# Optimization experiments

Measured on AMD Instinct MI355X. Metric: run time of the kernel, lower is better.

Reference implementation:

```python
import jax, jax.numpy as jnp
import numpy as np

B, S, E, H = 2, 2048, 1024, 16
D = E // H  # head_dim = 64

def setup_inputs() -> dict:
    key = jax.random.key(0)
    ks = jax.random.split(key, 5)
    scale = 0.02
    return {
        "x": jax.random.normal(ks[0], (B, S, E), dtype=jnp.float32),
        "Wq": jax.random.normal(ks[1], (E, E), dtype=jnp.float32) * scale,
        "Wk": jax.random.normal(ks[2], (E, E), dtype=jnp.float32) * scale,
        "Wv": jax.random.normal(ks[3], (E, E), dtype=jnp.float32) * scale,
        "Wo": jax.random.normal(ks[4], (E, E), dtype=jnp.float32) * scale,
        "bo": jnp.zeros((E,), dtype=jnp.float32),
    }

def reference(x, Wq, Wk, Wv, Wo, bo):
    b, s, e = x.shape
    # Linear projections (torch Linear: x @ W.T), split heads -> (b, h, s, d)
    q = (x @ Wq.T).reshape(b, s, H, D).transpose(0, 2, 1, 3)
    k = (x @ Wk.T).reshape(b, s, H, D).transpose(0, 2, 1, 3)
    v = (x @ Wv.T).reshape(b, s, H, D).transpose(0, 2, 1, 3)
    # Full materialized causal scores (b, h, s, s)
    scores = jnp.einsum("bhqd,bhkd->bhqk", q, k)
    causal = jnp.tril(jnp.ones((s, s), dtype=bool))  # True = keep
    scores = jnp.where(causal, scores, -jnp.inf)
    attn = jax.nn.softmax(scores / jnp.sqrt(jnp.float32(D)), axis=-1)
    ctx = jnp.einsum("bhqk,bhkd->bhqd", attn, v)
    ctx = ctx.transpose(0, 2, 1, 3).reshape(b, s, e)
    return ctx @ Wo.T + bo
```

## Files before the change

kernel.cpp:

```cpp
#include <hip/hip_runtime.h>
#include <hip/hip_bf16.h>

typedef __attribute__((ext_vector_type(8))) short short8_t;
typedef __attribute__((ext_vector_type(4))) short s4v;
typedef __attribute__((ext_vector_type(4))) float f32x4_t;
typedef __attribute__((ext_vector_type(4))) unsigned u32x4_t;
using u16 = unsigned short;

constexpr int S_LEN = 2048;
constexpr int EMB   = 1024;
constexpr int NH    = 16;
constexpr int HD    = 64;
constexpr int BATCH = 2;
constexpr int MR    = BATCH * S_LEN;
constexpr int E3    = 3 * EMB;

#define L2E 1.44269504f

__device__ __forceinline__ u16 f2bf(float f) {
  unsigned u = __builtin_bit_cast(unsigned, f);
  unsigned r = 0x7fffu + ((u >> 16) & 1u);
  return (u16)((u + r) >> 16);
}

__device__ __forceinline__ unsigned pkbf(float a, float b) {
  __hip_bfloat162 h = __float22bfloat162_rn(make_float2(a, b));
  unsigned u;
  __builtin_memcpy(&u, &h, 4);
  return u;
}

__device__ __forceinline__ void gld16(const void* g, void* l) {
  __builtin_amdgcn_global_load_lds(
      (const __attribute__((address_space(1))) void*)g,
      (__attribute__((address_space(3))) void*)l, 16, 0, 0);
}

template <int OFF>
__device__ __forceinline__ s4v tr16(const __attribute__((address_space(3))) u16* p) {
  s4v d;
  asm volatile("ds_read_b64_tr_b16 %0, %1 offset:%2"
               : "=v"(d) : "v"(p), "n"(OFF));
  return d;
}

__global__ void k_cvt_all(const float* __restrict__ x, const float* __restrict__ Wq,
                          const float* __restrict__ Wk, const float* __restrict__ Wv,
                          const float* __restrict__ Wo, u16* __restrict__ out) {
  int i = blockIdx.x * 256 + threadIdx.x;
  const float* src;
  int j;
  float sc = 1.0f;
  if (i < (1 << 20)) {
    src = x; j = i;
  } else {
    int jj = i - (1 << 20);
    int r = jj >> 18;
    j = jj & ((1 << 18) - 1);
    src = (r == 0) ? Wq : (r == 1) ? Wk : (r == 2) ? Wv : Wo;
    if (r == 0) sc = 0.125f;
  }
  float4 v = reinterpret_cast<const float4*>(src)[j];
  ushort4 o;
  o.x = f2bf(v.x * sc); o.y = f2bf(v.y * sc);
  o.z = f2bf(v.z * sc); o.w = f2bf(v.w * sc);
  reinterpret_cast<ushort4*>(out)[i] = o;
}

template <bool F32OUT>
__global__ __launch_bounds__(256) void k_gemm_bt(
    const u16* __restrict__ A, const u16* __restrict__ Bw,
    void* __restrict__ Cv, const float* __restrict__ bias,
    int M, int N, int K) {
  __shared__ short As[2][128 * 32];
  __shared__ short Bs[2][128 * 32];
  const int t    = threadIdx.x;
  const int w    = t >> 6;
  const int ln15 = t & 15;
  const int lg   = (t >> 4) & 3;
  const int wr   = w >> 1, wc = w & 1;

  const int nwgx = gridDim.x;
  const int lin  = blockIdx.y * nwgx + blockIdx.x;
  const int cpx  = (nwgx * gridDim.y) >> 3;
  const int lin2 = (lin & 7) * cpx + (lin >> 3);
  const int m0   = (lin2 / nwgx) * 128;
  const int n0   = (lin2 % nwgx) * 128;

  const int srow = t >> 2;
  const int scol = (t & 3) * 8;
  const u16* gA = A + (size_t)(m0 + srow) * K + scol;
  const u16* gB = Bw + (size_t)(n0 + srow) * K + scol;
  const int lofs = w * 512;

  f32x4_t acc[4][4] = {};

#define GSTAGE(buf, k0)                                                        \
  do {                                                                         \
    gld16(gA + (k0), &As[buf][lofs]);                                          \
    gld16(gA + (size_t)64 * K + (k0), &As[buf][lofs + 2048]);                  \
    gld16(gB + (k0), &Bs[buf][lofs]);                                          \
    gld16(gB + (size_t)64 * K + (k0), &Bs[buf][lofs + 2048]);                  \
  } while (0)

  const int nk = K >> 5;
  GSTAGE(0, 0);
  int cur = 0;

  for (int ki = 0; ki < nk; ++ki) {
    asm volatile("s_barrier" ::: "memory");
    if (ki + 1 < nk) {
      GSTAGE(cur ^ 1, (ki + 1) * 32);
      asm volatile("s_waitcnt vmcnt(4)" ::: "memory");
    } else {
      asm volatile("s_waitcnt vmcnt(0)" ::: "memory");
    }
    asm volatile("s_barrier" ::: "memory");

    short8_t af[4], bf[4];
#pragma unroll
    for (int i = 0; i < 4; ++i) {
      af[i] = *reinterpret_cast<const short8_t*>(
          &As[cur][(wr * 64 + i * 16 + ln15) * 32 + 8 * lg]);
      bf[i] = *reinterpret_cast<const short8_t*>(
          &Bs[cur][(wc * 64 + i * 16 + ln15) * 32 + 8 * lg]);
    }
#pragma unroll
    for (int i = 0; i < 4; ++i)
#pragma unroll
      for (int j = 0; j < 4; ++j)
        acc[i][j] = __builtin_amdgcn_mfma_f32_16x16x32_bf16(
            af[i], bf[j], acc[i][j], 0, 0, 0);
    cur ^= 1;
  }
#undef GSTAGE

  if (F32OUT) {
    float* C = reinterpret_cast<float*>(Cv);
#pragma unroll
    for (int i = 0; i < 4; ++i)
#pragma unroll
      for (int j = 0; j < 4; ++j) {
        const int col = n0 + wc * 64 + j * 16 + ln15;
        const float bv = bias ? bias[col] : 0.0f;
#pragma unroll
        for (int r = 0; r < 4; ++r) {
          const int row = m0 + wr * 64 + i * 16 + lg * 4 + r;
          C[(size_t)row * N + col] = acc[i][j][r] + bv;
        }
      }
  } else {
    u16* C = reinterpret_cast<u16*>(Cv);
#pragma unroll
    for (int i = 0; i < 4; ++i)
#pragma unroll
      for (int j = 0; j < 4; ++j) {
        const int col = n0 + wc * 64 + j * 16 + ln15;
#pragma unroll
        for (int r = 0; r < 4; ++r) {
          const int row = m0 + wr * 64 + i * 16 + lg * 4 + r;
          C[(size_t)row * N + col] = f2bf(acc[i][j][r]);
        }
      }
  }
}

__global__ __launch_bounds__(256, 4) void k_attn2(const u16* __restrict__ QKV,
                                                  u16* __restrict__ ctx) {
  __shared__ u16 Ks[2][64 * 64];
  __shared__ u16 Vs[2][64 * 64];

  const int t    = threadIdx.x;
  const int w    = t >> 6;
  const int l    = t & 63;
  const int ln15 = t & 15;
  const int lg   = (l >> 4) & 3;

  const int qt = 31 - blockIdx.y;
  const int bh = blockIdx.x;
  const int b  = bh >> 4, h = bh & 15;

  const u16* KVb = QKV + (size_t)b * S_LEN * E3 + h * HD;
  const u16* Kg  = KVb + 1024;
  const u16* Vg  = KVb + 2048;
  const int qrow = qt * 64 + w * 16;

  short8_t qf[2];
  {
    const u16* qp = KVb + (size_t)(qrow + ln15) * E3 + 8 * lg;
    qf[0] = *reinterpret_cast<const short8_t*>(qp);
    qf[1] = *reinterpret_cast<const short8_t*>(qp + 32);
  }

  const int krow_lo = l >> 3;
  const int kcol    = 8 * ((l & 7) ^ krow_lo);
  const int vkv     = l >> 1;
  const int vcol    = 16 * w + 8 * (l & 1);

  const int kx  = 8 * (ln15 & 7);
  const int kc0 = (8 * lg) ^ kx;
  const int kc1 = (32 + 8 * lg) ^ kx;

#define STAGE(buf, kv0)                                                        \
  do {                                                                         \
    gld16(Kg + (size_t)((kv0) + 16 * w + krow_lo) * E3 + kcol,                 \
          &Ks[buf][1024 * w]);                                                 \
    gld16(Kg + (size_t)((kv0) + 16 * w + 8 + krow_lo) * E3 + kcol,             \
          &Ks[buf][1024 * w + 512]);                                           \
    gld16(Vg + (size_t)((kv0) + vkv) * E3 + vcol, &Vs[buf][1024 * w]);         \
    gld16(Vg + (size_t)((kv0) + 32 + vkv) * E3 + vcol,                         \
          &Vs[buf][1024 * w + 512]);                                           \
  } while (0)

  f32x4_t o[4] = {};
  float mrow = -3e38f, lrow = 0.0f;
  const int nt_tiles = qt + 1;

  STAGE(0, 0);
  int cur = 0;

  for (int kvt = 0; kvt < nt_tiles; ++kvt) {
    const int kv0 = kvt * 64;
    asm volatile("s_barrier" ::: "memory");
    if (kvt + 1 < nt_tiles) {
      STAGE(cur ^ 1, kv0 + 64);
      asm volatile("s_waitcnt vmcnt(4)" ::: "memory");
    } else {
      asm volatile("s_waitcnt vmcnt(0)" ::: "memory");
    }
    asm volatile("s_barrier" ::: "memory");

    const __attribute__((address_space(3))) u16* vp =
        (const __attribute__((address_space(3))) u16*)&Vs[cur][4 * l];
    s4v vf[4][2][2];
#pragma unroll
    for (int nt = 0; nt < 4; ++nt) {
      if (nt == 0) { vf[0][0][0]=tr16<0>(vp);    vf[0][0][1]=tr16<512>(vp);
                     vf[0][1][0]=tr16<1024>(vp); vf[0][1][1]=tr16<1536>(vp); }
      if (nt == 1) { vf[1][0][0]=tr16<2048>(vp); vf[1][0][1]=tr16<2560>(vp);
                     vf[1][1][0]=tr16<3072>(vp); vf[1][1][1]=tr16<3584>(vp); }
      if (nt == 2) { vf[2][0][0]=tr16<4096>(vp); vf[2][0][1]=tr16<4608>(vp);
                     vf[2][1][0]=tr16<5120>(vp); vf[2][1][1]=tr16<5632>(vp); }
      if (nt == 3) { vf[3][0][0]=tr16<6144>(vp); vf[3][0][1]=tr16<6656>(vp);
                     vf[3][1][0]=tr16<7168>(vp); vf[3][1][1]=tr16<7680>(vp); }
    }

    f32x4_t tacc[4];
    __builtin_amdgcn_s_setprio(1);
#pragma unroll
    for (int ks = 0; ks < 4; ++ks) {
      const int R = 16 * ks + ln15;
      short8_t kf0 = *reinterpret_cast<const short8_t*>(&Ks[cur][R * 64 + kc0]);
      short8_t kf1 = *reinterpret_cast<const short8_t*>(&Ks[cur][R * 64 + kc1]);
      f32x4_t a = {0.f, 0.f, 0.f, 0.f};
      a = __builtin_amdgcn_mfma_f32_16x16x32_bf16(kf0, qf[0], a, 0, 0, 0);
      a = __builtin_amdgcn_mfma_f32_16x16x32_bf16(kf1, qf[1], a, 0, 0, 0);
      tacc[ks] = a;
    }
    __builtin_amdgcn_s_setprio(0);

    if (kvt == qt) {
      const int qg = qrow + ln15;
#pragma unroll
      for (int ks = 0; ks < 4; ++ks)
#pragma unroll
        for (int r = 0; r < 4; ++r)
          if (kv0 + 16 * ks + 4 * lg + r > qg) tacc[ks][r] = -3e38f;
    }

    float rm = fmaxf(
        fmaxf(fmaxf(fmaxf(tacc[0][0], tacc[0][1]), fmaxf(tacc[0][2], tacc[0][3])),
              fmaxf(fmaxf(tacc[1][0], tacc[1][1]), fmaxf(tacc[1][2], tacc[1][3]))),
        fmaxf(fmaxf(fmaxf(tacc[2][0], tacc[2][1]), fmaxf(tacc[2][2], tacc[2][3])),
              fmaxf(fmaxf(tacc[3][0], tacc[3][1]), fmaxf(tacc[3][2], tacc[3][3]))));
    rm = fmaxf(rm, __shfl_xor(rm, 16, 64));
    rm = fmaxf(rm, __shfl_xor(rm, 32, 64));

    if (__any(rm > mrow)) {
      const float nm = fmaxf(mrow, rm);
      const float sc = exp2f((mrow - nm) * L2E);
      mrow = nm;
      lrow *= sc;
#pragma unroll
      for (int r = 0; r < 4; ++r) {
        const float so = __shfl(sc, 20 * lg + r, 64);
#pragma unroll
        for (int nt = 0; nt < 4; ++nt) o[nt][r] *= so;
      }
    }

    const float nmL = mrow * L2E;
    float p[4][4];
    float rs = 0.0f;
#pragma unroll
    for (int ks = 0; ks < 4; ++ks)
#pragma unroll
      for (int r = 0; r < 4; ++r) {
        const float pv = exp2f(fmaf(tacc[ks][r], L2E, -nmL));
        p[ks][r] = pv;
        rs += pv;
      }
    rs += __shfl_xor(rs, 16, 64);
    rs += __shfl_xor(rs, 32, 64);
    lrow += rs;

    short8_t pf[2];
#pragma unroll
    for (int s2 = 0; s2 < 2; ++s2) {
      u32x4_t pu;
      pu[0] = pkbf(p[2 * s2][0], p[2 * s2][1]);
      pu[1] = pkbf(p[2 * s2][2], p[2 * s2][3]);
      pu[2] = pkbf(p[2 * s2 + 1][0], p[2 * s2 + 1][1]);
      pu[3] = pkbf(p[2 * s2 + 1][2], p[2 * s2 + 1][3]);
      pf[s2] = __builtin_bit_cast(short8_t, pu);
    }

    asm volatile("s_waitcnt lgkmcnt(0)");
    __builtin_amdgcn_sched_barrier(0);

    __builtin_amdgcn_s_setprio(1);
#pragma unroll
    for (int nt = 0; nt < 4; ++nt) {
#pragma unroll
      for (int s2 = 0; s2 < 2; ++s2) {
        short8_t bv = __builtin_shufflevector(vf[nt][s2][0], vf[nt][s2][1],
                                              0, 1, 2, 3, 4, 5, 6, 7);
        o[nt] = __builtin_amdgcn_mfma_f32_16x16x32_bf16(pf[s2], bv, o[nt], 0, 0, 0);
      }
    }
    __builtin_amdgcn_s_setprio(0);
    cur ^= 1;
  }
#undef STAGE

  const float linv = 1.0f / lrow;
#pragma unroll
  for (int r = 0; r < 4; ++r) {
    const float li = __shfl(linv, 20 * lg + r, 64);
    u16* op = ctx + (size_t)(b * S_LEN + qrow + 4 * lg + r) * EMB + h * HD;
#pragma unroll
    for (int nt = 0; nt < 4; ++nt)
      op[nt * 16 + ln15] = f2bf(o[nt][r] * li);
  }
}

extern "C" void kernel_launch(void* const* d_in, const int* in_sizes, int n_in,
                              void* d_out, int out_size, void* d_ws, size_t ws_size,
                              hipStream_t stream) {
  const float* x  = (const float*)d_in[0];
  const float* Wq = (const float*)d_in[1];
  const float* Wk = (const float*)d_in[2];
  const float* Wv = (const float*)d_in[3];
  const float* Wo = (const float*)d_in[4];
  const float* bo = (const float*)d_in[5];

  u16* ws   = (u16*)d_ws;
  u16* xb   = ws;
  u16* wcat = xb + (size_t)MR * EMB;
  u16* wob  = wcat + (size_t)3 * EMB * EMB;
  u16* qkv  = wob + (size_t)EMB * EMB;
  u16* ctxb = qkv + (size_t)MR * E3;

  k_cvt_all<<<8192, 256, 0, stream>>>(x, Wq, Wk, Wv, Wo, xb);

  k_gemm_bt<false><<<dim3(E3 / 128, MR / 128), 256, 0, stream>>>(
      xb, wcat, qkv, nullptr, MR, E3, EMB);

  k_attn2<<<dim3(BATCH * NH, 32), 256, 0, stream>>>(qkv, ctxb);

  k_gemm_bt<true><<<dim3(EMB / 128, MR / 128), 256, 0, stream>>>(
      ctxb, wob, d_out, bo, MR, EMB, EMB);
}
```

Baseline: 117.6 us.

## Process two KV tiles per iteration with a shared softmax rescale

Restructures the causal attention loop so each iteration loads and processes two 64-row KV tiles, computing a joint row max and rescaling the output once per 128 keys instead of once per 64. This roughly halves the per-tile softmax bookkeeping (max reduction shuffles, rescale of o) and the barrier count. It drops the double-buffered prefetch: both tiles are loaded and then waited on fully with vmcnt(0) before compute, so global loads no longer overlap compute. This exposes memory latency and adds register pressure from the second score tile.

Measured after the change: 122.1 us. 3.8% more time.

```diff
diff --git a/kernel.cpp b/kernel.cpp
--- a/kernel.cpp
+++ b/kernel.cpp
@@ -184,6 +184,7 @@
   const u16* Kg  = KVb + 1024;
   const u16* Vg  = KVb + 2048;
   const int qrow = qt * 64 + w * 16;
+  const int qg   = qrow + ln15;
 
   short8_t qf[2];
   {
@@ -212,67 +213,118 @@
           &Vs[buf][1024 * w + 512]);                                           \
   } while (0)
 
+#define VTRREAD(vf, buf)                                                       \
+  do {                                                                         \
+    const __attribute__((address_space(3))) u16* vp =                          \
+        (const __attribute__((address_space(3))) u16*)&Vs[buf][4 * l];         \
+    vf[0][0][0]=tr16<0>(vp);    vf[0][0][1]=tr16<512>(vp);                     \
+    vf[0][1][0]=tr16<1024>(vp); vf[0][1][1]=tr16<1536>(vp);                    \
+    vf[1][0][0]=tr16<2048>(vp); vf[1][0][1]=tr16<2560>(vp);                    \
+    vf[1][1][0]=tr16<3072>(vp); vf[1][1][1]=tr16<3584>(vp);                    \
+    vf[2][0][0]=tr16<4096>(vp); vf[2][0][1]=tr16<4608>(vp);                    \
+    vf[2][1][0]=tr16<5120>(vp); vf[2][1][1]=tr16<5632>(vp);                    \
+    vf[3][0][0]=tr16<6144>(vp); vf[3][0][1]=tr16<6656>(vp);                    \
+    vf[3][1][0]=tr16<7168>(vp); vf[3][1][1]=tr16<7680>(vp);                    \
+  } while (0)
+
+#define QKTILE(tacc, buf)                                                      \
+  do {                                                                         \
+    _Pragma("unroll")                                                          \
+    for (int ks = 0; ks < 4; ++ks) {                                           \
+      const int R = 16 * ks + ln15;                                            \
+      short8_t kf0 = *reinterpret_cast<const short8_t*>(&Ks[buf][R * 64 + kc0]);\
+      short8_t kf1 = *reinterpret_cast<const short8_t*>(&Ks[buf][R * 64 + kc1]);\
+      f32x4_t a = {0.f, 0.f, 0.f, 0.f};                                        \
+      a = __builtin_amdgcn_mfma_f32_16x16x32_bf16(kf0, qf[0], a, 0, 0, 0);     \
+      a = __builtin_amdgcn_mfma_f32_16x16x32_bf16(kf1, qf[1], a, 0, 0, 0);     \
+      tacc[ks] = a;                                                            \
+    }                                                                          \
+  } while (0)
+
+#define MASK(tacc, kvb)                                                        \
+  do {                                                                         \
+    _Pragma("unroll")                                                          \
+    for (int ks = 0; ks < 4; ++ks)                                             \
+      _Pragma("unroll")                                                        \
+      for (int r = 0; r < 4; ++r)                                              \
+        if ((kvb) + 16 * ks + 4 * lg + r > qg) tacc[ks][r] = -3e38f;           \
+  } while (0)
+
+#define EXPP(p, tacc)                                                          \
+  do {                                                                         \
+    _Pragma("unroll")                                                          \
+    for (int ks = 0; ks < 4; ++ks)                                             \
+      _Pragma("unroll")                                                        \
+      for (int r = 0; r < 4; ++r) {                                            \
+        const float pv = exp2f(fmaf(tacc[ks][r], L2E, -nmL));                  \
+        p[ks][r] = pv;                                                         \
+        rs += pv;                                                              \
+      }                                                                        \
+  } while (0)
+
+#define PACK(pf, p)                                                            \
+  do {                                                                         \
+    _Pragma("unroll")                                                          \
+    for (int s2 = 0; s2 < 2; ++s2) {                                           \
+      u32x4_t pu;                                                              \
+      pu[0] = pkbf(p[2 * s2][0], p[2 * s2][1]);                                \
+      pu[1] = pkbf(p[2 * s2][2], p[2 * s2][3]);                                \
+      pu[2] = pkbf(p[2 * s2 + 1][0], p[2 * s2 + 1][1]);                        \
+      pu[3] = pkbf(p[2 * s2 + 1][2], p[2 * s2 + 1][3]);                        \
+      pf[s2] = __builtin_bit_cast(short8_t, pu);                               \
+    }                                                                          \
+  } while (0)
+
+#define PV(pf, vf)                                                             \
+  do {                                                                         \
+    _Pragma("unroll")                                                          \
+    for (int nt = 0; nt < 4; ++nt)                                             \
+      _Pragma("unroll")                                                        \
+      for (int s2 = 0; s2 < 2; ++s2) {                                         \
+        short8_t bv = __builtin_shufflevector(vf[nt][s2][0], vf[nt][s2][1],    \
+                                              0, 1, 2, 3, 4, 5, 6, 7);         \
+        o[nt] = __builtin_amdgcn_mfma_f32_16x16x32_bf16(pf[s2], bv, o[nt],     \
+                                                        0, 0, 0);              \
+      }                                                                        \
+  } while (0)
+
   f32x4_t o[4] = {};
   float mrow = -3e38f, lrow = 0.0f;
-  const int nt_tiles = qt + 1;
-
-  STAGE(0, 0);
-  int cur = 0;
-
-  for (int kvt = 0; kvt < nt_tiles; ++kvt) {
-    const int kv0 = kvt * 64;
+
+  for (int kv0 = 0; kv0 <= qt * 64; kv0 += 128) {
+    const int t0   = kv0 >> 6;
+    const bool two = (t0 + 1 <= qt);
+
     asm volatile("s_barrier" ::: "memory");
-    if (kvt + 1 < nt_tiles) {
-      STAGE(cur ^ 1, kv0 + 64);
-      asm volatile("s_waitcnt vmcnt(4)" ::: "memory");
-    } else {
-      asm volatile("s_waitcnt vmcnt(0)" ::: "memory");
-    }
+    STAGE(0, kv0);
+    if (two) STAGE(1, kv0 + 64);
+    asm volatile("s_waitcnt vmcnt(0)" ::: "memory");
     asm volatile("s_barrier" ::: "memory");
 
-    const __attribute__((address_space(3))) u16* vp =
-        (const __attribute__((address_space(3))) u16*)&Vs[cur][4 * l];
-    s4v vf[4][2][2];
-#pragma unroll
-    for (int nt = 0; nt < 4; ++nt) {
-      if (nt == 0) { vf[0][0][0]=tr16<0>(vp);    vf[0][0][1]=tr16<512>(vp);
-                     vf[0][1][0]=tr16<1024>(vp); vf[0][1][1]=tr16<1536>(vp); }
-      if (nt == 1) { vf[1][0][0]=tr16<2048>(vp); vf[1][0][1]=tr16<2560>(vp);
-                     vf[1][1][0]=tr16<3072>(vp); vf[1][1][1]=tr16<3584>(vp); }
-      if (nt == 2) { vf[2][0][0]=tr16<4096>(vp); vf[2][0][1]=tr16<4608>(vp);
-                     vf[2][1][0]=tr16<5120>(vp); vf[2][1][1]=tr16<5632>(vp); }
-      if (nt == 3) { vf[3][0][0]=tr16<6144>(vp); vf[3][0][1]=tr16<6656>(vp);
-                     vf[3][1][0]=tr16<7168>(vp); vf[3][1][1]=tr16<7680>(vp); }
-    }
-
-    f32x4_t tacc[4];
+    s4v vfA[4][2][2];
+    VTRREAD(vfA, 0);
+
+    f32x4_t ta[4], tb[4];
     __builtin_amdgcn_s_setprio(1);
-#pragma unroll
-    for (int ks = 0; ks < 4; ++ks) {
-      const int R = 16 * ks + ln15;
-      short8_t kf0 = *reinterpret_cast<const short8_t*>(&Ks[cur][R * 64 + kc0]);
-      short8_t kf1 = *reinterpret_cast<const short8_t*>(&Ks[cur][R * 64 + kc1]);
-      f32x4_t a = {0.f, 0.f, 0.f, 0.f};
-      a = __builtin_amdgcn_mfma_f32_16x16x32_bf16(kf0, qf[0], a, 0, 0, 0);
-      a = __builtin_amdgcn_mfma_f32_16x16x32_bf16(kf1, qf[1], a, 0, 0, 0);
-      tacc[ks] = a;
-    }
+    QKTILE(ta, 0);
+    if (two) QKTILE(tb, 1);
     __builtin_amdgcn_s_setprio(0);
 
-    if (kvt == qt) {
-      const int qg = qrow + ln15;
-#pragma unroll
-      for (int ks = 0; ks < 4; ++ks)
-#pragma unroll
-        for (int r = 0; r < 4; ++r)
-          if (kv0 + 16 * ks + 4 * lg + r > qg) tacc[ks][r] = -3e38f;
-    }
+    if (!two) MASK(ta, kv0);
+    if (two && (t0 + 1 == qt)) MASK(tb, kv0 + 64);
 
     float rm = fmaxf(
-        fmaxf(fmaxf(fmaxf(tacc[0][0], tacc[0][1]), fmaxf(tacc[0][2], tacc[0][3])),
-              fmaxf(fmaxf(tacc[1][0], tacc[1][1]), fmaxf(tacc[1][2], tacc[1][3]))),
-        fmaxf(fmaxf(fmaxf(tacc[2][0], tacc[2][1]), fmaxf(tacc[2][2], tacc[2][3])),
-              fmaxf(fmaxf(tacc[3][0], tacc[3][1]), fmaxf(tacc[3][2], tacc[3][3]))));
+        fmaxf(fmaxf(fmaxf(ta[0][0], ta[0][1]), fmaxf(ta[0][2], ta[0][3])),
+              fmaxf(fmaxf(ta[1][0], ta[1][1]), fmaxf(ta[1][2], ta[1][3]))),
+        fmaxf(fmaxf(fmaxf(ta[2][0], ta[2][1]), fmaxf(ta[2][2], ta[2][3])),
+              fmaxf(fmaxf(ta[3][0], ta[3][1]), fmaxf(ta[3][2], ta[3][3]))));
+    if (two) {
+      rm = fmaxf(rm, fmaxf(
+          fmaxf(fmaxf(fmaxf(tb[0][0], tb[0][1]), fmaxf(tb[0][2], tb[0][3])),
+                fmaxf(fmaxf(tb[1][0], tb[1][1]), fmaxf(tb[1][2], tb[1][3]))),
+          fmaxf(fmaxf(fmaxf(tb[2][0], tb[2][1]), fmaxf(tb[2][2], tb[2][3])),
+                fmaxf(fmaxf(tb[3][0], tb[3][1]), fmaxf(tb[3][2], tb[3][3])))));
+    }
     rm = fmaxf(rm, __shfl_xor(rm, 16, 64));
     rm = fmaxf(rm, __shfl_xor(rm, 32, 64));
 
@@ -290,48 +342,44 @@
     }
 
     const float nmL = mrow * L2E;
-    float p[4][4];
     float rs = 0.0f;
-#pragma unroll
-    for (int ks = 0; ks < 4; ++ks)
-#pragma unroll
-      for (int r = 0; r < 4; ++r) {
-        const float pv = exp2f(fmaf(tacc[ks][r], L2E, -nmL));
-        p[ks][r] = pv;
-        rs += pv;
-      }
+    float pA[4][4];
+    EXPP(pA, ta);
+    short8_t pfA[2];
+    PACK(pfA, pA);
+    short8_t pfB[2];
+    if (two) {
+      float pB[4][4];
+      EXPP(pB, tb);
+      PACK(pfB, pB);
+    }
     rs += __shfl_xor(rs, 16, 64);
     rs += __shfl_xor(rs, 32, 64);
     lrow += rs;
 
-    short8_t pf[2];
-#pragma unroll
-    for (int s2 = 0; s2 < 2; ++s2) {
-      u32x4_t pu;
-      pu[0] = pkbf(p[2 * s2][0], p[2 * s2][1]);
-      pu[1] = pkbf(p[2 * s2][2], p[2 * s2][3]);
-      pu[2] = pkbf(p[2 * s2 + 1][0], p[2 * s2 + 1][1]);
-      pu[3] = pkbf(p[2 * s2 + 1][2], p[2 * s2 + 1][3]);
-      pf[s2] = __builtin_bit_cast(short8_t, pu);
-    }
-
     asm volatile("s_waitcnt lgkmcnt(0)");
     __builtin_amdgcn_sched_barrier(0);
-
     __builtin_amdgcn_s_setprio(1);
-#pragma unroll
-    for (int nt = 0; nt < 4; ++nt) {
-#pragma unroll
-      for (int s2 = 0; s2 < 2; ++s2) {
-        short8_t bv = __builtin_shufflevector(vf[nt][s2][0], vf[nt][s2][1],
-                                              0, 1, 2, 3, 4, 5, 6, 7);
-        o[nt] = __builtin_amdgcn_mfma_f32_16x16x32_bf16(pf[s2], bv, o[nt], 0, 0, 0);
-      }
-    }
+    PV(pfA, vfA);
     __builtin_amdgcn_s_setprio(0);
-    cur ^= 1;
+
+    if (two) {
+      s4v vfB[4][2][2];
+      VTRREAD(vfB, 1);
+      asm volatile("s_waitcnt lgkmcnt(0)");
+      __builtin_amdgcn_sched_barrier(0);
+      __builtin_amdgcn_s_setprio(1);
+      PV(pfB, vfB);
+      __builtin_amdgcn_s_setprio(0);
+    }
   }
 #undef STAGE
+#undef VTRREAD
+#undef QKTILE
+#undef MASK
+#undef EXPP
+#undef PACK
+#undef PV
 
   const float linv = 1.0f / lrow;
 #pragma unroll
```

## Use 256x256-tile 512-thread GEMM kernel for QKV projection

Applied to the files above, without the earlier changes.

Adds a new bf16 MFMA GEMM kernel with 256x256 output tiles, 8 waves, K-step 64 and double-buffered LDS with XOR swizzle, and uses it for the fused QKV projection instead of the 128x128 kernel. Larger tiles raise arithmetic intensity and cut global/L2 traffic per FLOP. The cost is a 12x16=192-workgroup grid, which gives lower occupancy (one block per CU, 128KB LDS) and may under-fill the CUs. It also carries a large register footprint from the 32 accumulators per lane.

After: 119.7 us. No clear change (+1.9%).

```diff
diff --git a/kernel.cpp b/kernel.cpp
--- a/kernel.cpp
+++ b/kernel.cpp
@@ -67,6 +67,103 @@
   reinterpret_cast<ushort4*>(out)[i] = o;
 }
 
+__global__ __launch_bounds__(512, 1) void k_gemm256(
+    const u16* __restrict__ A, const u16* __restrict__ Bw,
+    u16* __restrict__ C, int M, int N) {
+  constexpr int K = 1024;
+  __shared__ u16 Ab[2][16384];
+  __shared__ u16 Bb[2][16384];
+
+  const int t    = threadIdx.x;
+  const int ww   = t >> 6;
+  const int l    = t & 63;
+  const int ln15 = t & 15;
+  const int lg   = (t >> 4) & 3;
+  const int wr   = ww >> 2;
+  const int wc   = ww & 3;
+
+  const int nwgx = gridDim.x;
+  const int lin  = blockIdx.y * nwgx + blockIdx.x;
+  const int cpx  = (nwgx * gridDim.y) >> 3;
+  const int lin2 = (lin & 7) * cpx + (lin >> 3);
+  const int m0   = (lin2 / nwgx) * 256;
+  const int n0   = (lin2 % nwgx) * 256;
+
+  const int srow = t >> 3;
+  const int rlo  = (t >> 3) & 7;
+  const int scol = 8 * ((t & 7) ^ rlo);
+
+  const int kx  = 8 * (ln15 & 7);
+  const int kc0 = (8 * lg) ^ kx;
+  const int kc1 = (32 + 8 * lg) ^ kx;
+
+  f32x4_t acc[8][4] = {};
+
+#define GST256(buf, ki)                                                        \
+  do {                                                                         \
+    _Pragma("unroll")                                                          \
+    for (int i = 0; i < 4; ++i)                                                \
+      gld16(A + (size_t)(m0 + 64 * i + srow) * K + 64 * (ki) + scol,           \
+            &Ab[buf][i * 4096 + ww * 512]);                                    \
+    _Pragma("unroll")                                                          \
+    for (int i = 0; i < 4; ++i)                                                \
+      gld16(Bw + (size_t)(n0 + 64 * i + srow) * K + 64 * (ki) + scol,          \
+            &Bb[buf][i * 4096 + ww * 512]);                                    \
+  } while (0)
+
+  constexpr int nk = K / 64;
+  GST256(0, 0);
+  int cur = 0;
+
+  for (int ki = 0; ki < nk; ++ki) {
+    asm volatile("s_barrier" ::: "memory");
+    if (ki + 1 < nk) {
+      GST256(cur ^ 1, ki + 1);
+      asm volatile("s_waitcnt vmcnt(8)" ::: "memory");
+    } else {
+      asm volatile("s_waitcnt vmcnt(0)" ::: "memory");
+    }
+    asm volatile("s_barrier" ::: "memory");
+
+#pragma unroll
+    for (int kh = 0; kh < 2; ++kh) {
+      const int kc = kh ? kc1 : kc0;
+      short8_t af[8], bf[4];
+#pragma unroll
+      for (int mi = 0; mi < 8; ++mi)
+        af[mi] = *reinterpret_cast<const short8_t*>(
+            &Ab[cur][(wr * 128 + 16 * mi + ln15) * 64 + kc]);
+#pragma unroll
+      for (int ni = 0; ni < 4; ++ni)
+        bf[ni] = *reinterpret_cast<const short8_t*>(
+            &Bb[cur][(wc * 64 + 16 * ni + ln15) * 64 + kc]);
+      __builtin_amdgcn_s_setprio(1);
+#pragma unroll
+      for (int mi = 0; mi < 8; ++mi)
+#pragma unroll
+        for (int ni = 0; ni < 4; ++ni)
+          acc[mi][ni] = __builtin_amdgcn_mfma_f32_16x16x32_bf16(
+              af[mi], bf[ni], acc[mi][ni], 0, 0, 0);
+      __builtin_amdgcn_s_setprio(0);
+    }
+    cur ^= 1;
+  }
+#undef GST256
+
+#pragma unroll
+  for (int mi = 0; mi < 8; ++mi) {
+#pragma unroll
+    for (int ni = 0; ni < 4; ++ni) {
+      const int col = n0 + wc * 64 + 16 * ni + ln15;
+#pragma unroll
+      for (int rr = 0; rr < 4; ++rr) {
+        const int row = m0 + wr * 128 + 16 * mi + 4 * lg + rr;
+        C[(size_t)row * N + col] = f2bf(acc[mi][ni][rr]);
+      }
+    }
+  }
+}
+
 template <bool F32OUT>
 __global__ __launch_bounds__(256) void k_gemm_bt(
     const u16* __restrict__ A, const u16* __restrict__ Bw,
@@ -363,8 +460,8 @@
 
   k_cvt_all<<<8192, 256, 0, stream>>>(x, Wq, Wk, Wv, Wo, xb);
 
-  k_gemm_bt<false><<<dim3(E3 / 128, MR / 128), 256, 0, stream>>>(
-      xb, wcat, qkv, nullptr, MR, E3, EMB);
+  k_gemm256<<<dim3(E3 / 256, MR / 256), 512, 0, stream>>>(
+      xb, wcat, qkv, MR, E3);
 
   k_attn2<<<dim3(BATCH * NH, 32), 256, 0, stream>>>(qkv, ctxb);
 
```

## Split KV tiles across two wave groups per attention block and merge

Applied to the files above, without the earlier changes.

The attention block grows to 512 threads, split into two groups of four waves. Each group processes alternating KV tiles for the same 64 query rows, and the partial softmax states are merged through shared memory at the end. This halves the serial KV loop per block and raises in-flight waves. In exchange, each group drops its double-buffered prefetch and waits with vmcnt(0) every iteration, so load latency is no longer hidden. It also adds a shared-memory merge step, and the 512-thread launch bound may tighten the per-thread register budget.

Result: slower. 122.7 us (+4.4%).

```diff
diff --git a/kernel.cpp b/kernel.cpp
--- a/kernel.cpp
+++ b/kernel.cpp
@@ -165,17 +165,21 @@
   }
 }
 
-__global__ __launch_bounds__(256, 4) void k_attn2(const u16* __restrict__ QKV,
+__global__ __launch_bounds__(512, 4) void k_attn2(const u16* __restrict__ QKV,
                                                   u16* __restrict__ ctx) {
-  __shared__ u16 Ks[2][64 * 64];
-  __shared__ u16 Vs[2][64 * 64];
+  __shared__ u16 sh[16384];
 
   const int t    = threadIdx.x;
   const int w    = t >> 6;
+  const int g    = w >> 2;
+  const int wg   = w & 3;
   const int l    = t & 63;
   const int ln15 = t & 15;
   const int lg   = (l >> 4) & 3;
 
+  u16* Ksg = sh + g * 4096;
+  u16* Vsg = sh + 8192 + g * 4096;
+
   const int qt = 31 - blockIdx.y;
   const int bh = blockIdx.x;
   const int b  = bh >> 4, h = bh & 15;
@@ -183,7 +187,7 @@
   const u16* KVb = QKV + (size_t)b * S_LEN * E3 + h * HD;
   const u16* Kg  = KVb + 1024;
   const u16* Vg  = KVb + 2048;
-  const int qrow = qt * 64 + w * 16;
+  const int qrow = qt * 64 + wg * 16;
 
   short8_t qf[2];
   {
@@ -195,63 +199,53 @@
   const int krow_lo = l >> 3;
   const int kcol    = 8 * ((l & 7) ^ krow_lo);
   const int vkv     = l >> 1;
-  const int vcol    = 16 * w + 8 * (l & 1);
+  const int vcol    = 16 * wg + 8 * (l & 1);
 
   const int kx  = 8 * (ln15 & 7);
   const int kc0 = (8 * lg) ^ kx;
   const int kc1 = (32 + 8 * lg) ^ kx;
 
-#define STAGE(buf, kv0)                                                        \
-  do {                                                                         \
-    gld16(Kg + (size_t)((kv0) + 16 * w + krow_lo) * E3 + kcol,                 \
-          &Ks[buf][1024 * w]);                                                 \
-    gld16(Kg + (size_t)((kv0) + 16 * w + 8 + krow_lo) * E3 + kcol,             \
-          &Ks[buf][1024 * w + 512]);                                           \
-    gld16(Vg + (size_t)((kv0) + vkv) * E3 + vcol, &Vs[buf][1024 * w]);         \
-    gld16(Vg + (size_t)((kv0) + 32 + vkv) * E3 + vcol,                         \
-          &Vs[buf][1024 * w + 512]);                                           \
-  } while (0)
-
   f32x4_t o[4] = {};
   float mrow = -3e38f, lrow = 0.0f;
-  const int nt_tiles = qt + 1;
-
-  STAGE(0, 0);
-  int cur = 0;
-
-  for (int kvt = 0; kvt < nt_tiles; ++kvt) {
-    const int kv0 = kvt * 64;
+  const int nIter = (qt >> 1) + 1;
+
+  for (int it = 0; it < nIter; ++it) {
+    const int kvt  = 2 * it + g;
+    const bool have = (kvt <= qt);
+    const int kv0  = kvt * 64;
+
     asm volatile("s_barrier" ::: "memory");
-    if (kvt + 1 < nt_tiles) {
-      STAGE(cur ^ 1, kv0 + 64);
-      asm volatile("s_waitcnt vmcnt(4)" ::: "memory");
-    } else {
-      asm volatile("s_waitcnt vmcnt(0)" ::: "memory");
-    }
+    if (have) {
+      gld16(Kg + (size_t)(kv0 + 16 * wg + krow_lo) * E3 + kcol, &Ksg[1024 * wg]);
+      gld16(Kg + (size_t)(kv0 + 16 * wg + 8 + krow_lo) * E3 + kcol,
+            &Ksg[1024 * wg + 512]);
+      gld16(Vg + (size_t)(kv0 + vkv) * E3 + vcol, &Vsg[1024 * wg]);
+      gld16(Vg + (size_t)(kv0 + 32 + vkv) * E3 + vcol, &Vsg[1024 * wg + 512]);
+    }
+    asm volatile("s_waitcnt vmcnt(0)" ::: "memory");
     asm volatile("s_barrier" ::: "memory");
 
+    if (!have) continue;
+
     const __attribute__((address_space(3))) u16* vp =
-        (const __attribute__((address_space(3))) u16*)&Vs[cur][4 * l];
+        (const __attribute__((address_space(3))) u16*)&Vsg[4 * l];
     s4v vf[4][2][2];
-#pragma unroll
-    for (int nt = 0; nt < 4; ++nt) {
-      if (nt == 0) { vf[0][0][0]=tr16<0>(vp);    vf[0][0][1]=tr16<512>(vp);
-                     vf[0][1][0]=tr16<1024>(vp); vf[0][1][1]=tr16<1536>(vp); }
-      if (nt == 1) { vf[1][0][0]=tr16<2048>(vp); vf[1][0][1]=tr16<2560>(vp);
-                     vf[1][1][0]=tr16<3072>(vp); vf[1][1][1]=tr16<3584>(vp); }
-      if (nt == 2) { vf[2][0][0]=tr16<4096>(vp); vf[2][0][1]=tr16<4608>(vp);
-                     vf[2][1][0]=tr16<5120>(vp); vf[2][1][1]=tr16<5632>(vp); }
-      if (nt == 3) { vf[3][0][0]=tr16<6144>(vp); vf[3][0][1]=tr16<6656>(vp);
-                     vf[3][1][0]=tr16<7168>(vp); vf[3][1][1]=tr16<7680>(vp); }
-    }
+    vf[0][0][0]=tr16<0>(vp);    vf[0][0][1]=tr16<512>(vp);
+    vf[0][1][0]=tr16<1024>(vp); vf[0][1][1]=tr16<1536>(vp);
+    vf[1][0][0]=tr16<2048>(vp); vf[1][0][1]=tr16<2560>(vp);
+    vf[1][1][0]=tr16<3072>(vp); vf[1][1][1]=tr16<3584>(vp);
+    vf[2][0][0]=tr16<4096>(vp); vf[2][0][1]=tr16<4608>(vp);
+    vf[2][1][0]=tr16<5120>(vp); vf[2][1][1]=tr16<5632>(vp);
+    vf[3][0][0]=tr16<6144>(vp); vf[3][0][1]=tr16<6656>(vp);
+    vf[3][1][0]=tr16<7168>(vp); vf[3][1][1]=tr16<7680>(vp);
 
     f32x4_t tacc[4];
     __builtin_amdgcn_s_setprio(1);
 #pragma unroll
     for (int ks = 0; ks < 4; ++ks) {
       const int R = 16 * ks + ln15;
-      short8_t kf0 = *reinterpret_cast<const short8_t*>(&Ks[cur][R * 64 + kc0]);
-      short8_t kf1 = *reinterpret_cast<const short8_t*>(&Ks[cur][R * 64 + kc1]);
+      short8_t kf0 = *reinterpret_cast<const short8_t*>(&Ksg[R * 64 + kc0]);
+      short8_t kf1 = *reinterpret_cast<const short8_t*>(&Ksg[R * 64 + kc1]);
       f32x4_t a = {0.f, 0.f, 0.f, 0.f};
       a = __builtin_amdgcn_mfma_f32_16x16x32_bf16(kf0, qf[0], a, 0, 0, 0);
       a = __builtin_amdgcn_mfma_f32_16x16x32_bf16(kf1, qf[1], a, 0, 0, 0);
@@ -329,18 +323,42 @@
       }
     }
     __builtin_amdgcn_s_setprio(0);
-    cur ^= 1;
-  }
-#undef STAGE
-
-  const float linv = 1.0f / lrow;
-#pragma unroll
-  for (int r = 0; r < 4; ++r) {
-    const float li = __shfl(linv, 20 * lg + r, 64);
-    u16* op = ctx + (size_t)(b * S_LEN + qrow + 4 * lg + r) * EMB + h * HD;
+  }
+
+  asm volatile("s_barrier" ::: "memory");
+  float* sm = (float*)sh;
+  const int sidx = t & 255;
+  if (g == 1) {
 #pragma unroll
     for (int nt = 0; nt < 4; ++nt)
-      op[nt * 16 + ln15] = f2bf(o[nt][r] * li);
+#pragma unroll
+      for (int r = 0; r < 4; ++r) sm[sidx * 18 + nt * 4 + r] = o[nt][r];
+    sm[sidx * 18 + 16] = mrow;
+    sm[sidx * 18 + 17] = lrow;
+  }
+  asm volatile("s_waitcnt lgkmcnt(0)" ::: "memory");
+  asm volatile("s_barrier" ::: "memory");
+
+  if (g == 0) {
+    const float m1 = sm[sidx * 18 + 16];
+    const float l1 = sm[sidx * 18 + 17];
+    const float mm = fmaxf(mrow, m1);
+    const float w0 = exp2f((mrow - mm) * L2E);
+    const float w1 = exp2f((m1 - mm) * L2E);
+    const float lt = lrow * w0 + l1 * w1;
+    const float linv = 1.0f / lt;
+#pragma unroll
+    for (int r = 0; r < 4; ++r) {
+      const float a0 = __shfl(w0, 20 * lg + r, 64);
+      const float a1 = __shfl(w1, 20 * lg + r, 64);
+      const float li = __shfl(linv, 20 * lg + r, 64);
+      u16* op = ctx + (size_t)(b * S_LEN + qrow + 4 * lg + r) * EMB + h * HD;
+#pragma unroll
+      for (int nt = 0; nt < 4; ++nt) {
+        const float om = o[nt][r] * a0 + sm[sidx * 18 + nt * 4 + r] * a1;
+        op[nt * 16 + ln15] = f2bf(om * li);
+      }
+    }
   }
 }
 
@@ -366,7 +384,7 @@
   k_gemm_bt<false><<<dim3(E3 / 128, MR / 128), 256, 0, stream>>>(
       xb, wcat, qkv, nullptr, MR, E3, EMB);
 
-  k_attn2<<<dim3(BATCH * NH, 32), 256, 0, stream>>>(qkv, ctxb);
+  k_attn2<<<dim3(BATCH * NH, 32), 512, 0, stream>>>(qkv, ctxb);
 
   k_gemm_bt<true><<<dim3(EMB / 128, MR / 128), 256, 0, stream>>>(
       ctxb, wob, d_out, bo, MR, EMB, EMB);
```
